# Kernel tuning notes

Hardware: AMD Instinct MI355X
Metric: run time of the kernel (lower is better)

Reference implementation:

```python
import jax, jax.numpy as jnp
import numpy as np

MIN_BIN_WIDTH = 1e-3
MIN_BIN_HEIGHT = 1e-3
MIN_DERIVATIVE = 1e-3
TAIL_BOUND = 1.0
N_POS = 2097152
N_CHANNELS = 8
N_BINS = 128
DEFAULT_INIT = float(np.log(np.exp(1.0 - MIN_DERIVATIVE) - 1.0))


def setup_inputs() -> dict:
    key = jax.random.key(0)
    k1, k2, k3, k4 = jax.random.split(key, 4)
    # positions rescaled to roughly [-1, 1]; include slight tail overshoot
    x = jax.random.uniform(k1, (N_POS, N_CHANNELS), minval=-1.1, maxval=1.1, dtype=jnp.float32)
    uw = DEFAULT_INIT + 0.1 * jax.random.normal(k2, (N_CHANNELS, N_BINS), dtype=jnp.float32)
    uh = DEFAULT_INIT + 0.1 * jax.random.normal(k3, (N_CHANNELS, N_BINS), dtype=jnp.float32)
    ud = DEFAULT_INIT + 0.1 * jax.random.normal(k4, (N_CHANNELS, N_BINS - 1), dtype=jnp.float32)
    return {"x": x, "unnormalized_widths": uw, "unnormalized_heights": uh,
            "unnormalized_derivatives": ud}


def _bin_edges(unnormalized, min_size, left, right):
    # softmax-normalized sizes with a minimum bin size, cumsum -> knot locations
    n_bins = unnormalized.shape[-1]
    sizes = jax.nn.softmax(unnormalized, axis=-1)
    sizes = min_size + (1.0 - min_size * n_bins) * sizes
    cum = jnp.cumsum(sizes, axis=-1)
    cum = jnp.pad(cum, ((0, 0), (1, 0)))
    cum = (right - left) * cum + left
    cum = cum.at[..., 0].set(left).at[..., -1].set(right)
    sizes = cum[..., 1:] - cum[..., :-1]
    return sizes, cum


def _log_prob(x, uw, uh, ud):
    left, right = -TAIL_BOUND, TAIL_BOUND
    bottom, top = -TAIL_BOUND, TAIL_BOUND
    C = uw.shape[0]

    widths, cumwidths = _bin_edges(uw * 10.0, MIN_BIN_WIDTH, left, right)      # (C,B),(C,B+1)
    heights, cumheights = _bin_edges(uh * 10.0, MIN_BIN_HEIGHT, bottom, top)   # (C,B),(C,B+1)
    ud_pad = jnp.pad(ud, ((0, 0), (1, 1)), constant_values=DEFAULT_INIT)       # linear tails
    derivatives = MIN_DERIVATIVE + jax.nn.softplus(ud_pad)                      # (C,B+1)
    delta = heights / widths                                                    # (C,B)

    inside = (x >= left) & (x <= right)
    xc = jnp.clip(x, bottom, top)  # inverse pass searches over cumheights

    edges = cumheights.at[:, -1].add(1e-6)
    # per-channel bin search, memory-light searchsorted
    idx = jax.vmap(lambda e, v: jnp.searchsorted(e, v, side='right'),
                   in_axes=(0, 1), out_axes=1)(edges, xc) - 1                   # (N,C)
    idx = jnp.clip(idx, 0, widths.shape[-1] - 1)

    ch = jnp.arange(C)[None, :]
    icw = cumwidths[ch, idx]
    ibw = widths[ch, idx]
    ich = cumheights[ch, idx]
    ih = heights[ch, idx]
    idl = delta[ch, idx]
    d0 = derivatives[ch, idx]
    d1 = derivatives[ch, idx + 1]

    # quadratic inverse solve (Durkan et al. rational-quadratic spline)
    dy = xc - ich
    t = d0 + d1 - 2.0 * idl
    a = dy * t + ih * (idl - d0)
    b = ih * d0 - dy * t
    c = -idl * dy
    disc = jnp.maximum(b * b - 4.0 * a * c, 0.0)
    root = (2.0 * c) / (-b - jnp.sqrt(disc))
    theta_1m = root * (1.0 - root)
    denom = idl + t * theta_1m
    der_num = (idl ** 2) * (d1 * root ** 2 + 2.0 * idl * theta_1m + d0 * (1.0 - root) ** 2)
    logabsdet = jnp.log(der_num) - 2.0 * jnp.log(denom)
    logdet = jnp.where(inside, -logabsdet, 0.0)  # identity tails -> logdet 0
    return np.log(0.5).astype(np.float32) + logdet


def reference(x, unnormalized_widths, unnormalized_heights, unnormalized_derivatives):
    return _log_prob(x, unnormalized_widths, unnormalized_heights, unnormalized_derivatives)
```

## Files before the change

kernel.cpp:

```cpp
#include <hip/hip_runtime.h>
#include <math.h>


#define NB 128
#define NCH 8
#define NSLOT 1024
#define EP_F 0
#define P4_F 2064
#define HINT_F 6192
#define TAB_FLOATS 8240

__global__ __launch_bounds__(128) void spline_precompute(
    const float* __restrict__ uw, const float* __restrict__ uh,
    const float* __restrict__ ud, float* __restrict__ ws)
{
    const int c = blockIdx.x;
    const int i = threadIdx.x;
    __shared__ float red[128];
    __shared__ float scan[128];
    __shared__ float cum[129];
    __shared__ float wdt[128];
    __shared__ float sdv[129];
    const float DEFAULT_INIT = logf(expf(1.0f - 1e-3f) - 1.0f);

    float v = uw[c * NB + i] * 10.0f;
    red[i] = v; __syncthreads();
    #pragma unroll
    for (int s = 64; s >= 1; s >>= 1) { if (i < s) red[i] = fmaxf(red[i], red[i + s]); __syncthreads(); }
    float ex = expf(v - red[0]);
    __syncthreads();
    red[i] = ex; __syncthreads();
    #pragma unroll
    for (int s = 64; s >= 1; s >>= 1) { if (i < s) red[i] += red[i + s]; __syncthreads(); }
    float sz = 1e-3f + (1.0f - 1e-3f * NB) * (ex / red[0]);
    __syncthreads();
    scan[i] = sz;
    for (int off = 1; off < NB; off <<= 1) {
        __syncthreads();
        float t = (i >= off) ? scan[i - off] : 0.0f;
        __syncthreads();
        scan[i] += t;
    }
    __syncthreads();
    if (i == 0) cum[0] = -1.0f;
    cum[i + 1] = (i == NB - 1) ? 1.0f : fmaf(2.0f, scan[i], -1.0f);
    __syncthreads();
    wdt[i] = cum[i + 1] - cum[i];
    __syncthreads();

    v = uh[c * NB + i] * 10.0f;
    red[i] = v; __syncthreads();
    #pragma unroll
    for (int s = 64; s >= 1; s >>= 1) { if (i < s) red[i] = fmaxf(red[i], red[i + s]); __syncthreads(); }
    ex = expf(v - red[0]);
    __syncthreads();
    red[i] = ex; __syncthreads();
    #pragma unroll
    for (int s = 64; s >= 1; s >>= 1) { if (i < s) red[i] += red[i + s]; __syncthreads(); }
    sz = 1e-3f + (1.0f - 1e-3f * NB) * (ex / red[0]);
    __syncthreads();
    scan[i] = sz;
    for (int off = 1; off < NB; off <<= 1) {
        __syncthreads();
        float t = (i >= off) ? scan[i - off] : 0.0f;
        __syncthreads();
        scan[i] += t;
    }
    __syncthreads();
    if (i == 0) cum[0] = -1.0f;
    cum[i + 1] = (i == NB - 1) ? 1.0f : fmaf(2.0f, scan[i], -1.0f);

    float u0 = (i == 0) ? DEFAULT_INIT : ud[c * (NB - 1) + i - 1];
    sdv[i] = 1e-3f + log1pf(expf(u0));
    if (i == NB - 1) sdv[NB] = 1e-3f + log1pf(expf(DEFAULT_INIT));
    __syncthreads();

    float hh  = cum[i + 1] - cum[i];
    float idl = hh / wdt[i];
    const int o = c * 129 + i;
    float2* g_ep = reinterpret_cast<float2*>(ws + EP_F);
    float4* g_p4 = reinterpret_cast<float4*>(ws + P4_F);

    float e1 = (i == NB - 1) ? (1.0f + 1e-6f) : cum[i + 1];
    g_ep[o] = make_float2(cum[i], e1);
    g_p4[o] = make_float4(hh, idl, sdv[i], sdv[i + 1]);
    if (i == NB - 1) {
        g_ep[o + 1] = make_float2(1.0f, 1.0f + 1e-6f);
        g_p4[o + 1] = make_float4(1.0f, 1.0f, 1.0f, 1.0f);
    }

    unsigned char* g_hint = reinterpret_cast<unsigned char*>(ws + HINT_F);
    for (int s = i; s < NSLOT; s += NB) {
        float left = (float)s * (2.0f / NSLOT) - 1.0f;
        int k = 0;
        #pragma unroll
        for (int st = 64; st >= 1; st >>= 1) {
            int t = k + st;
            if (cum[t] <= left) k = t;
        }
        g_hint[c * NSLOT + s] = (unsigned char)k;
    }
}

__global__ __launch_bounds__(256, 4) void spline_main(
    const float4* __restrict__ x4, float4* __restrict__ out4,
    const float* __restrict__ ws, int npair)
{
    __shared__ __align__(16) float tab[TAB_FLOATS];
    {
        float4* dst = reinterpret_cast<float4*>(tab);
        const float4* src = reinterpret_cast<const float4*>(ws);
        for (int t = threadIdx.x; t < TAB_FLOATS / 4; t += 256) dst[t] = src[t];
    }
    __syncthreads();
    const float2* ep = reinterpret_cast<const float2*>(tab + EP_F);
    const float4* p4 = reinterpret_cast<const float4*>(tab + P4_F);
    const unsigned char* hint = reinterpret_cast<const unsigned char*>(tab + HINT_F);

    const float LOG_HALF = -0.6931471805599453f;
    const float LN2 = 0.6931471805599453f;
    const int tid = blockIdx.x * 256 + threadIdx.x;
    const int stride = gridDim.x * 256;

    float4 pfa = x4[2 * tid];
    float4 pfb = x4[2 * tid + 1];

    for (int i = tid; i < npair; i += stride) {
        float4 xa = pfa, xb = pfb;
        int inx = i + stride;
        inx = (inx < npair) ? inx : i;
        pfa = x4[2 * inx];
        pfb = x4[2 * inx + 1];

        float xs[8] = {xa.x, xa.y, xa.z, xa.w, xb.x, xb.y, xb.z, xb.w};

        float xq[8];
        int kk[8];
        #pragma unroll
        for (int j = 0; j < 8; ++j) {
            float xc = fminf(fmaxf(xs[j], -1.0f), 1.0f);
            xq[j] = xc;
            int s = (int)fmaf(xc, (float)(NSLOT / 2), (float)(NSLOT / 2));
            s = (s > NSLOT - 1) ? NSLOT - 1 : s;
            kk[j] = hint[j * NSLOT + s];
        }

        float2 ee[8];
        #pragma unroll
        for (int j = 0; j < 8; ++j) ee[j] = ep[j * 129 + kk[j]];

        float4 pk[8];
        float dyv[8], lm[8];
        #pragma unroll
        for (int j = 0; j < 8; ++j) {
            bool adv = (ee[j].y <= xq[j]);
            int k2 = kk[j] + (adv ? 1 : 0);
            float ich = adv ? ee[j].y : ee[j].x;
            dyv[j] = xq[j] - ich;
            lm[j] = (xs[j] == xq[j]) ? LN2 : 0.0f;
            pk[j] = p4[j * 129 + k2];
        }

        float rs[8];
        #pragma unroll
        for (int j = 0; j < 8; ++j) {
            float h = pk[j].x, dl = pk[j].y, d0 = pk[j].z, d1 = pk[j].w;
            float dy = dyv[j];

            float T   = fmaf(-2.0f, dl, d0 + d1);
            float dyt = dy * T;
            float B   = h * d0;
            float A   = fmaf(h, dl, -B);
            float aa  = dyt + A;
            float bb  = B - dyt;
            float cc  = -dl * dy;
            float ac  = aa * cc;
            float disc = fmaxf(fmaf(-4.0f, ac, bb * bb), 0.0f);
            float sq  = __builtin_amdgcn_sqrtf(disc);
            float w   = -bb - sq;
            float u   = cc + cc;
            float w2  = w * w;
            float tu  = T * u;
            float sdd = dl - d0;
            float E   = sdd + sdd;
            float t1  = fmaf(E, w, tu);
            float num = fmaf(t1, u, d0 * w2);
            float d2  = dl * dl;
            float numf = (num * w2) * d2;
            float wmu = w - u;
            float denb = fmaf(tu, wmu, dl * w2);
            float den2 = denb * denb;
            float val = __fdividef(numf, den2);
            rs[j] = fmaf(-lm[j], __log2f(val), LOG_HALF);
        }

        out4[2 * i]     = make_float4(rs[0], rs[1], rs[2], rs[3]);
        out4[2 * i + 1] = make_float4(rs[4], rs[5], rs[6], rs[7]);
    }
}

extern "C" void kernel_launch(void* const* d_in, const int* in_sizes, int n_in,
                              void* d_out, int out_size, void* d_ws, size_t ws_size,
                              hipStream_t stream) {
    const float* x  = (const float*)d_in[0];
    const float* uw = (const float*)d_in[1];
    const float* uh = (const float*)d_in[2];
    const float* ud = (const float*)d_in[3];
    float* ws = (float*)d_ws;

    spline_precompute<<<NCH, NB, 0, stream>>>(uw, uh, ud, ws);

    const int npair = out_size / 8;
    spline_main<<<1024, 256, 0, stream>>>(
        (const float4*)x, (float4*)d_out, ws, npair);
}
```

Baseline: 44.82 us.

## Pack spline math into float2 vectors, shrink edge table, widen grid

Result: faster. 42.42 us (-5.4%).

```diff
diff --git a/kernel.cpp b/kernel.cpp
--- a/kernel.cpp
+++ b/kernel.cpp
@@ -5,10 +5,12 @@
 #define NB 128
 #define NCH 8
 #define NSLOT 1024
-#define EP_F 0
-#define P4_F 2064
-#define HINT_F 6192
-#define TAB_FLOATS 8240
+#define E_F 0
+#define P4_F 1032
+#define HINT_F 5160
+#define TAB_FLOATS 7208
+
+typedef float v2f __attribute__((ext_vector_type(2)));
 
 __global__ __launch_bounds__(128) void spline_precompute(
     const float* __restrict__ uw, const float* __restrict__ uh,
@@ -78,16 +80,11 @@
     float hh  = cum[i + 1] - cum[i];
     float idl = hh / wdt[i];
     const int o = c * 129 + i;
-    float2* g_ep = reinterpret_cast<float2*>(ws + EP_F);
+
+    ws[E_F + o] = cum[i];
+    if (i == NB - 1) ws[E_F + c * 129 + NB] = 1.0f + 1e-6f;
     float4* g_p4 = reinterpret_cast<float4*>(ws + P4_F);
-
-    float e1 = (i == NB - 1) ? (1.0f + 1e-6f) : cum[i + 1];
-    g_ep[o] = make_float2(cum[i], e1);
     g_p4[o] = make_float4(hh, idl, sdv[i], sdv[i + 1]);
-    if (i == NB - 1) {
-        g_ep[o + 1] = make_float2(1.0f, 1.0f + 1e-6f);
-        g_p4[o + 1] = make_float4(1.0f, 1.0f, 1.0f, 1.0f);
-    }
 
     unsigned char* g_hint = reinterpret_cast<unsigned char*>(ws + HINT_F);
     for (int s = i; s < NSLOT; s += NB) {
@@ -113,7 +110,7 @@
         for (int t = threadIdx.x; t < TAB_FLOATS / 4; t += 256) dst[t] = src[t];
     }
     __syncthreads();
-    const float2* ep = reinterpret_cast<const float2*>(tab + EP_F);
+    const float* eg = tab + E_F;
     const float4* p4 = reinterpret_cast<const float4*>(tab + P4_F);
     const unsigned char* hint = reinterpret_cast<const unsigned char*>(tab + HINT_F);
 
@@ -122,8 +119,8 @@
     const int tid = blockIdx.x * 256 + threadIdx.x;
     const int stride = gridDim.x * 256;
 
-    float4 pfa = x4[2 * tid];
-    float4 pfb = x4[2 * tid + 1];
+    float4 pfa, pfb;
+    if (tid < npair) { pfa = x4[2 * tid]; pfb = x4[2 * tid + 1]; }
 
     for (int i = tid; i < npair; i += stride) {
         float4 xa = pfa, xb = pfb;
@@ -145,17 +142,21 @@
             kk[j] = hint[j * NSLOT + s];
         }
 
-        float2 ee[8];
-        #pragma unroll
-        for (int j = 0; j < 8; ++j) ee[j] = ep[j * 129 + kk[j]];
+        float e0[8], e1[8];
+        #pragma unroll
+        for (int j = 0; j < 8; ++j) {
+            const float* ej = eg + j * 129 + kk[j];
+            e0[j] = ej[0];
+            e1[j] = ej[1];
+        }
 
         float4 pk[8];
         float dyv[8], lm[8];
         #pragma unroll
         for (int j = 0; j < 8; ++j) {
-            bool adv = (ee[j].y <= xq[j]);
+            bool adv = (e1[j] <= xq[j]);
             int k2 = kk[j] + (adv ? 1 : 0);
-            float ich = adv ? ee[j].y : ee[j].x;
+            float ich = adv ? e1[j] : e0[j];
             dyv[j] = xq[j] - ich;
             lm[j] = (xs[j] == xq[j]) ? LN2 : 0.0f;
             pk[j] = p4[j * 129 + k2];
@@ -163,35 +164,46 @@
 
         float rs[8];
         #pragma unroll
-        for (int j = 0; j < 8; ++j) {
-            float h = pk[j].x, dl = pk[j].y, d0 = pk[j].z, d1 = pk[j].w;
-            float dy = dyv[j];
-
-            float T   = fmaf(-2.0f, dl, d0 + d1);
-            float dyt = dy * T;
-            float B   = h * d0;
-            float A   = fmaf(h, dl, -B);
-            float aa  = dyt + A;
-            float bb  = B - dyt;
-            float cc  = -dl * dy;
-            float ac  = aa * cc;
-            float disc = fmaxf(fmaf(-4.0f, ac, bb * bb), 0.0f);
-            float sq  = __builtin_amdgcn_sqrtf(disc);
-            float w   = -bb - sq;
-            float u   = cc + cc;
-            float w2  = w * w;
-            float tu  = T * u;
-            float sdd = dl - d0;
-            float E   = sdd + sdd;
-            float t1  = fmaf(E, w, tu);
-            float num = fmaf(t1, u, d0 * w2);
-            float d2  = dl * dl;
-            float numf = (num * w2) * d2;
-            float wmu = w - u;
-            float denb = fmaf(tu, wmu, dl * w2);
-            float den2 = denb * denb;
-            float val = __fdividef(numf, den2);
-            rs[j] = fmaf(-lm[j], __log2f(val), LOG_HALF);
+        for (int jj = 0; jj < 4; ++jj) {
+            v2f h  = {pk[jj].x, pk[jj + 4].x};
+            v2f dl = {pk[jj].y, pk[jj + 4].y};
+            v2f d0 = {pk[jj].z, pk[jj + 4].z};
+            v2f d1 = {pk[jj].w, pk[jj + 4].w};
+            v2f dy = {dyv[jj],  dyv[jj + 4]};
+            const v2f m2 = {-2.0f, -2.0f};
+            const v2f m4 = {-4.0f, -4.0f};
+            const v2f zz = {0.0f, 0.0f};
+
+            v2f T    = __builtin_elementwise_fma(m2, dl, d0 + d1);
+            v2f dyt  = dy * T;
+            v2f B    = h * d0;
+            v2f A    = __builtin_elementwise_fma(h, dl, -B);
+            v2f aa   = dyt + A;
+            v2f bb   = B - dyt;
+            v2f cc   = -dl * dy;
+            v2f ac   = aa * cc;
+            v2f disc = __builtin_elementwise_max(
+                           __builtin_elementwise_fma(m4, ac, bb * bb), zz);
+            v2f sq   = {__builtin_amdgcn_sqrtf(disc.x),
+                        __builtin_amdgcn_sqrtf(disc.y)};
+            v2f w    = -bb - sq;
+            v2f u    = cc + cc;
+            v2f w2   = w * w;
+            v2f tu   = T * u;
+            v2f sdd  = dl - d0;
+            v2f E    = sdd + sdd;
+            v2f t1   = __builtin_elementwise_fma(E, w, tu);
+            v2f num  = __builtin_elementwise_fma(t1, u, d0 * w2);
+            v2f d2   = dl * dl;
+            v2f numf = (num * w2) * d2;
+            v2f wmu  = w - u;
+            v2f denb = __builtin_elementwise_fma(tu, wmu, dl * w2);
+            v2f den2 = denb * denb;
+
+            float va = __fdividef(numf.x, den2.x);
+            float vb = __fdividef(numf.y, den2.y);
+            rs[jj]     = fmaf(-lm[jj],     __log2f(va), LOG_HALF);
+            rs[jj + 4] = fmaf(-lm[jj + 4], __log2f(vb), LOG_HALF);
         }
 
         out4[2 * i]     = make_float4(rs[0], rs[1], rs[2], rs[3]);
@@ -211,6 +223,6 @@
     spline_precompute<<<NCH, NB, 0, stream>>>(uw, uh, ud, ws);
 
     const int npair = out_size / 8;
-    spline_main<<<1024, 256, 0, stream>>>(
+    spline_main<<<1280, 256, 0, stream>>>(
         (const float4*)x, (float4*)d_out, ws, npair);
 }
```
